# Kernel tuning notes

Measured on AMD Instinct MI355X. Metric: run time of the kernel, lower is better.

Reference implementation:

```python
import jax, jax.numpy as jnp
import numpy as np

B, INPUT_DIM, OUTPUT_DIM, Z_DIM = 32, 2048, 2048, 64
NNZ = 209715


def setup_inputs() -> dict:
    key = jax.random.key(0)
    k_x, k_z, k_w, k_b = jax.random.split(key, 4)
    x = jax.random.normal(k_x, (B, INPUT_DIM), dtype=jnp.float32)
    z = jax.random.normal(k_z, (B, Z_DIM), dtype=jnp.float32)
    W_net = jax.random.normal(k_w, (Z_DIM, NNZ), dtype=jnp.float32) * 0.02
    b_net = jax.random.normal(k_b, (NNZ,), dtype=jnp.float32) * 0.02
    # unique nonzero positions of output_matrix [INPUT_DIM, OUTPUT_DIM]
    rng = np.random.default_rng(0)
    lin = rng.choice(INPUT_DIM * OUTPUT_DIM, size=NNZ, replace=False)
    in_idx = jnp.asarray(lin // OUTPUT_DIM, dtype=jnp.int32)   # rows  -> input dim
    out_idx = jnp.asarray(lin % OUTPUT_DIM, dtype=jnp.int32)   # cols  -> output dim
    return {"x": x, "z": z, "W_net": W_net, "b_net": b_net,
            "in_idx": in_idx, "out_idx": out_idx}


def reference(x, z, W_net, b_net, in_idx, out_idx):
    # hypernetwork: net(z) -> [B, NNZ] matrix entries
    mat_entity = z @ W_net + b_net                      # [B, NNZ]
    # scatter into zero-filled dense matrix: mat[:, out_idx, in_idx] = entries
    mat = jnp.zeros((x.shape[0], OUTPUT_DIM, INPUT_DIM), dtype=x.dtype)
    mat = mat.at[:, out_idx, in_idx].set(mat_entity)    # [B, O, I]
    # batched matvec
    return jnp.einsum('boi,bi->bo', mat, x)             # [B, O]
```

## Files before the change

kernel.cpp:

```cpp
#include <hip/hip_runtime.h>
#include <hip/hip_bf16.h>

#define BATCH   32
#define IN_DIM  2048
#define OUT_DIM 2048
#define ZDIM    64
#define NNZ     209715
#define CAP     160
#define TILES   ((NNZ + 15) / 16)
#define CBLOCKS ((TILES + 3) / 4)
#define NBLK    ((NNZ + 1023) / 1024)

typedef __attribute__((ext_vector_type(8))) short bf16x8;
typedef __attribute__((ext_vector_type(4))) float f32x4;

#define OFF_XT   0
#define OFF_ZBF  262144
#define OFF_CNT  270336
#define OFF_BH   278528
#define OFF_ROW  2375680
#define OFF_E    3214592
#define B_WS_NEEDED (OFF_E + (size_t)OUT_DIM * CAP * BATCH * 2)

__device__ __forceinline__ short f2bf(float f) {
    unsigned u = __float_as_uint(f);
    u += 0x7fffu + ((u >> 16) & 1u);
    return (short)(u >> 16);
}

__global__ __launch_bounds__(256) void prep_x(
    const float* __restrict__ x, const float* __restrict__ z,
    float* __restrict__ xT, short* __restrict__ zbf)
{
    const int idx = blockIdx.x * 256 + threadIdx.x;
    const int b = idx >> 11;
    const int i = idx & 2047;
    xT[i * BATCH + b] = x[idx];
    if (idx < BATCH * ZDIM) zbf[idx] = f2bf(z[idx]);
}

__global__ __launch_bounds__(1024) void hist_blk(
    const int* __restrict__ out_idx, int* __restrict__ bh)
{
    __shared__ int lh[OUT_DIM];
    const int t = threadIdx.x, blk = blockIdx.x;
    lh[t] = 0; lh[t + 1024] = 0;
    __syncthreads();
    const int k = blk * 1024 + t;
    if (k < NNZ) atomicAdd(&lh[out_idx[k]], 1);
    __syncthreads();
    bh[t * 256 + blk]          = lh[t];
    bh[(t + 1024) * 256 + blk] = lh[t + 1024];
}

__global__ __launch_bounds__(256) void colscan(
    int* __restrict__ bh, int* __restrict__ cnt)
{
    const int o    = blockIdx.x * 4 + (threadIdx.x >> 6);
    const int lane = threadIdx.x & 63;
    const int i0   = lane * 4;
    int4 v = *reinterpret_cast<int4*>(bh + o * 256 + i0);
    const int a = (i0 + 0 < NBLK) ? v.x : 0;
    const int b = (i0 + 1 < NBLK) ? v.y : 0;
    const int c = (i0 + 2 < NBLK) ? v.z : 0;
    const int d = (i0 + 3 < NBLK) ? v.w : 0;
    const int s1 = a + b, s2 = s1 + c, tot = s2 + d;
    int inc = tot;
    #pragma unroll
    for (int t = 1; t < 64; t <<= 1) {
        const int n = __shfl_up(inc, t);
        if (lane >= t) inc += n;
    }
    const int exc = inc - tot;
    int4 w; w.x = exc; w.y = exc + a; w.z = exc + s1; w.w = exc + s2;
    *reinterpret_cast<int4*>(bh + o * 256 + i0) = w;
    if (lane == 63) cnt[o] = inc;
}

__global__ __launch_bounds__(1024) void slot_blk(
    const int* __restrict__ out_idx, const int* __restrict__ bh,
    int* __restrict__ rowOf)
{
    __shared__ int lh[OUT_DIM];
    const int t = threadIdx.x, blk = blockIdx.x;
    lh[t] = 0; lh[t + 1024] = 0;
    __syncthreads();
    const int k = blk * 1024 + t;
    if (k < NNZ) {
        const int oi  = out_idx[k];
        const int r   = atomicAdd(&lh[oi], 1);
        const int pos = bh[oi * 256 + blk] + r;
        rowOf[k] = (pos < CAP) ? oi * CAP + pos : -1;
    }
}

__global__ __launch_bounds__(256, 4) void compute_mfma(
    const short* __restrict__ zbf, const float* __restrict__ W,
    const float* __restrict__ bn, const int* __restrict__ in_idx,
    const int* __restrict__ rowOf, const float* __restrict__ xT,
    short* __restrict__ E)
{
    const int lane = threadIdx.x & 63;
    const int m    = lane & 15;
    const int hi   = lane >> 4;
    const int t    = blockIdx.x * 4 + (threadIdx.x >> 6);
    if (t >= TILES) return;
    const int k0 = t * 16;

    bf16x8 zf[2][2];
    #pragma unroll
    for (int bt = 0; bt < 2; ++bt)
        #pragma unroll
        for (int jt = 0; jt < 2; ++jt)
            zf[bt][jt] = *reinterpret_cast<const bf16x8*>(
                zbf + (bt * 16 + m) * ZDIM + jt * 32 + hi * 8);

    const int kA = (k0 + m < NNZ) ? (k0 + m) : (NNZ - 1);
    const float* wp = W + (size_t)(hi * 8) * NNZ + kA;
    float wv[16];
    #pragma unroll
    for (int e = 0; e < 8; ++e) wv[e]     = wp[(size_t)e * NNZ];
    #pragma unroll
    for (int e = 0; e < 8; ++e) wv[8 + e] = wp[(size_t)(32 + e) * NNZ];

    int rowL = -1, iiL = 0; float bnL = 0.f;
    if (lane < 16) {
        const int kk = k0 + lane;
        if (kk < NNZ) {
            rowL = rowOf[kk];
            iiL  = in_idx[kk];
            bnL  = bn[kk];
        }
    }

    union { bf16x8 v; short s[8]; } a0, a1;
    #pragma unroll
    for (int e = 0; e < 8; ++e) { a0.s[e] = f2bf(wv[e]); a1.s[e] = f2bf(wv[8 + e]); }

    f32x4 acc0 = {0.f, 0.f, 0.f, 0.f};
    f32x4 acc1 = {0.f, 0.f, 0.f, 0.f};
    acc0 = __builtin_amdgcn_mfma_f32_16x16x32_bf16(a0.v, zf[0][0], acc0, 0, 0, 0);
    acc0 = __builtin_amdgcn_mfma_f32_16x16x32_bf16(a1.v, zf[0][1], acc0, 0, 0, 0);
    acc1 = __builtin_amdgcn_mfma_f32_16x16x32_bf16(a0.v, zf[1][0], acc1, 0, 0, 0);
    acc1 = __builtin_amdgcn_mfma_f32_16x16x32_bf16(a1.v, zf[1][1], acc1, 0, 0, 0);

    #pragma unroll
    for (int r = 0; r < 4; ++r) {
        const int src  = hi * 4 + r;
        const int row  = __shfl(rowL, src);
        const int ii   = __shfl(iiL, src);
        const float bb = __shfl(bnL, src);
        if (row >= 0) {
            const float x0 = xT[ii * BATCH + m];
            const float x1 = xT[ii * BATCH + 16 + m];
            short* Ep = E + (size_t)row * BATCH;
            Ep[m]      = f2bf((acc0[r] + bb) * x0);
            Ep[16 + m] = f2bf((acc1[r] + bb) * x1);
        }
    }
}

__global__ __launch_bounds__(256) void reduce_bf16(
    const short* __restrict__ E, const int* __restrict__ cnt,
    float* __restrict__ out)
{
    __shared__ float partial[2][BATCH];
    const int wave = threadIdx.x >> 6;
    const int lane = threadIdx.x & 63;
    const int cs   = wave >> 1;
    const int part = wave & 1;
    const int o    = blockIdx.x * 2 + cs;
    const int r  = lane >> 2;
    const int bg = lane & 3;
    const int s = o * CAP;
    int c = cnt[o]; if (c > CAP) c = CAP;
    const int e = s + c;

    float acc[8];
    #pragma unroll
    for (int q = 0; q < 8; ++q) acc[q] = 0.f;

    for (int p = s + part * 16 + r; p < e; p += 32) {
        const uint4 v = *reinterpret_cast<const uint4*>(E + (size_t)p * BATCH + bg * 8);
        const unsigned u[4] = {v.x, v.y, v.z, v.w};
        #pragma unroll
        for (int q = 0; q < 4; ++q) {
            acc[2 * q]     += __uint_as_float((u[q] & 0xFFFFu) << 16);
            acc[2 * q + 1] += __uint_as_float(u[q] & 0xFFFF0000u);
        }
    }

    #pragma unroll
    for (int d = 4; d < 64; d <<= 1)
        #pragma unroll
        for (int q = 0; q < 8; ++q)
            acc[q] += __shfl_xor(acc[q], d);

    if (part == 1 && lane < 4) {
        #pragma unroll
        for (int q = 0; q < 8; ++q) partial[cs][bg * 8 + q] = acc[q];
    }
    __syncthreads();
    if (part == 0 && lane < 4) {
        #pragma unroll
        for (int q = 0; q < 8; ++q)
            out[(bg * 8 + q) * OUT_DIM + o] = acc[q] + partial[cs][bg * 8 + q];
    }
}

__global__ __launch_bounds__(256) void hyper_scatter_kernel(
    const float* __restrict__ x, const float* __restrict__ z,
    const float* __restrict__ W, const float* __restrict__ bn,
    const int* __restrict__ in_idx, const int* __restrict__ out_idx,
    float* __restrict__ out)
{
    __shared__ float zs[BATCH * ZDIM];
    const int tid = threadIdx.x;
    {
        const float4* zg  = reinterpret_cast<const float4*>(z);
        float4*       zsv = reinterpret_cast<float4*>(zs);
        zsv[tid]       = zg[tid];
        zsv[tid + 256] = zg[tid + 256];
    }
    __syncthreads();
    const int k = blockIdx.x * 256 + tid;
    if (k >= NNZ) return;
    float w[ZDIM];
    #pragma unroll
    for (int j = 0; j < ZDIM; ++j) w[j] = W[(size_t)j * NNZ + k];
    const float bk = bn[k];
    const int ii = in_idx[k], oi = out_idx[k];
    const float4* zv = reinterpret_cast<const float4*>(zs);
    #pragma unroll
    for (int b = 0; b < BATCH; ++b) {
        float e = bk;
        #pragma unroll
        for (int j4 = 0; j4 < ZDIM / 4; ++j4) {
            const float4 zz = zv[b * (ZDIM / 4) + j4];
            e = fmaf(zz.x, w[j4 * 4 + 0], e);
            e = fmaf(zz.y, w[j4 * 4 + 1], e);
            e = fmaf(zz.z, w[j4 * 4 + 2], e);
            e = fmaf(zz.w, w[j4 * 4 + 3], e);
        }
        atomicAdd(&out[b * OUT_DIM + oi], e * x[b * IN_DIM + ii]);
    }
}

extern "C" void kernel_launch(void* const* d_in, const int* in_sizes, int n_in,
                              void* d_out, int out_size, void* d_ws, size_t ws_size,
                              hipStream_t stream) {
    const float* x       = (const float*)d_in[0];
    const float* z       = (const float*)d_in[1];
    const float* W       = (const float*)d_in[2];
    const float* bn      = (const float*)d_in[3];
    const int*   in_idx  = (const int*)d_in[4];
    const int*   out_idx = (const int*)d_in[5];
    float*       out     = (float*)d_out;
    char*        ws      = (char*)d_ws;

    if (ws_size >= B_WS_NEEDED) {
        float* xT    = (float*)(ws + OFF_XT);
        short* zbf   = (short*)(ws + OFF_ZBF);
        int*   cnt   = (int*)(ws + OFF_CNT);
        int*   bh    = (int*)(ws + OFF_BH);
        int*   rowOf = (int*)(ws + OFF_ROW);
        short* E     = (short*)(ws + OFF_E);

        prep_x   <<<(BATCH * IN_DIM) / 256, 256, 0, stream>>>(x, z, xT, zbf);
        hist_blk <<<NBLK, 1024, 0, stream>>>(out_idx, bh);
        colscan  <<<OUT_DIM / 4, 256, 0, stream>>>(bh, cnt);
        slot_blk <<<NBLK, 1024, 0, stream>>>(out_idx, bh, rowOf);
        compute_mfma<<<CBLOCKS, 256, 0, stream>>>(zbf, W, bn, in_idx, rowOf, xT, E);
        reduce_bf16 <<<OUT_DIM / 2, 256, 0, stream>>>(E, cnt, out);
    } else {
        hipMemsetAsync(out, 0, (size_t)BATCH * OUT_DIM * sizeof(float), stream);
        const int grid = (NNZ + 255) / 256;
        hyper_scatter_kernel<<<grid, 256, 0, stream>>>(x, z, W, bn, in_idx, out_idx, out);
    }
}
```

Baseline: 46.32 us.

## Fuse x-prep into histogram, process two tiles per wave, one wave per output reduce

Merges the x-transpose/z-conversion kernel into the histogram kernel so one launch goes away. The MFMA compute kernel now handles two 16-entry tiles per wave and issues all W, index and x loads before the matrix ops, to expose more memory-level parallelism. The reduce kernel switches from two waves per output column with an LDS combine and barrier to one wave per column. The costs are higher register pressure in the compute kernel and less parallelism per column in the reduce.

```diff
diff --git a/kernel.cpp b/kernel.cpp
--- a/kernel.cpp
+++ b/kernel.cpp
@@ -8,7 +8,9 @@
 #define NNZ     209715
 #define CAP     160
 #define TILES   ((NNZ + 15) / 16)
-#define CBLOCKS ((TILES + 3) / 4)
+#define TPW     2
+#define CWAVES  ((TILES + TPW - 1) / TPW)
+#define CBLOCKS ((CWAVES + 3) / 4)
 #define NBLK    ((NNZ + 1023) / 1024)
 
 typedef __attribute__((ext_vector_type(8))) short bf16x8;
@@ -28,26 +30,22 @@
     return (short)(u >> 16);
 }
 
-__global__ __launch_bounds__(256) void prep_x(
-    const float* __restrict__ x, const float* __restrict__ z,
+__global__ __launch_bounds__(1024) void hist_prep(
+    const int* __restrict__ out_idx, const float* __restrict__ x,
+    const float* __restrict__ z, int* __restrict__ bh,
     float* __restrict__ xT, short* __restrict__ zbf)
-{
-    const int idx = blockIdx.x * 256 + threadIdx.x;
-    const int b = idx >> 11;
-    const int i = idx & 2047;
-    xT[i * BATCH + b] = x[idx];
-    if (idx < BATCH * ZDIM) zbf[idx] = f2bf(z[idx]);
-}
-
-__global__ __launch_bounds__(1024) void hist_blk(
-    const int* __restrict__ out_idx, int* __restrict__ bh)
 {
     __shared__ int lh[OUT_DIM];
     const int t = threadIdx.x, blk = blockIdx.x;
     lh[t] = 0; lh[t + 1024] = 0;
     __syncthreads();
-    const int k = blk * 1024 + t;
-    if (k < NNZ) atomicAdd(&lh[out_idx[k]], 1);
+    const int gid = blk * 1024 + t;
+    if (gid < BATCH * IN_DIM) {
+        const int b = gid >> 11, i = gid & 2047;
+        xT[i * BATCH + b] = x[gid];
+        if (gid < BATCH * ZDIM) zbf[gid] = f2bf(z[gid]);
+    }
+    if (gid < NNZ) atomicAdd(&lh[out_idx[gid]], 1);
     __syncthreads();
     bh[t * 256 + blk]          = lh[t];
     bh[(t + 1024) * 256 + blk] = lh[t + 1024];
@@ -103,9 +101,9 @@
     const int lane = threadIdx.x & 63;
     const int m    = lane & 15;
     const int hi   = lane >> 4;
-    const int t    = blockIdx.x * 4 + (threadIdx.x >> 6);
-    if (t >= TILES) return;
-    const int k0 = t * 16;
+    const int wid  = blockIdx.x * 4 + (threadIdx.x >> 6);
+    const int t0   = wid * TPW;
+    if (t0 >= TILES) return;
 
     bf16x8 zf[2][2];
     #pragma unroll
@@ -115,47 +113,64 @@
             zf[bt][jt] = *reinterpret_cast<const bf16x8*>(
                 zbf + (bt * 16 + m) * ZDIM + jt * 32 + hi * 8);
 
-    const int kA = (k0 + m < NNZ) ? (k0 + m) : (NNZ - 1);
-    const float* wp = W + (size_t)(hi * 8) * NNZ + kA;
-    float wv[16];
-    #pragma unroll
-    for (int e = 0; e < 8; ++e) wv[e]     = wp[(size_t)e * NNZ];
-    #pragma unroll
-    for (int e = 0; e < 8; ++e) wv[8 + e] = wp[(size_t)(32 + e) * NNZ];
-
-    int rowL = -1, iiL = 0; float bnL = 0.f;
-    if (lane < 16) {
-        const int kk = k0 + lane;
-        if (kk < NNZ) {
-            rowL = rowOf[kk];
-            iiL  = in_idx[kk];
-            bnL  = bn[kk];
-        }
-    }
-
-    union { bf16x8 v; short s[8]; } a0, a1;
-    #pragma unroll
-    for (int e = 0; e < 8; ++e) { a0.s[e] = f2bf(wv[e]); a1.s[e] = f2bf(wv[8 + e]); }
-
-    f32x4 acc0 = {0.f, 0.f, 0.f, 0.f};
-    f32x4 acc1 = {0.f, 0.f, 0.f, 0.f};
-    acc0 = __builtin_amdgcn_mfma_f32_16x16x32_bf16(a0.v, zf[0][0], acc0, 0, 0, 0);
-    acc0 = __builtin_amdgcn_mfma_f32_16x16x32_bf16(a1.v, zf[0][1], acc0, 0, 0, 0);
-    acc1 = __builtin_amdgcn_mfma_f32_16x16x32_bf16(a0.v, zf[1][0], acc1, 0, 0, 0);
-    acc1 = __builtin_amdgcn_mfma_f32_16x16x32_bf16(a1.v, zf[1][1], acc1, 0, 0, 0);
-
-    #pragma unroll
-    for (int r = 0; r < 4; ++r) {
-        const int src  = hi * 4 + r;
-        const int row  = __shfl(rowL, src);
-        const int ii   = __shfl(iiL, src);
-        const float bb = __shfl(bnL, src);
-        if (row >= 0) {
-            const float x0 = xT[ii * BATCH + m];
-            const float x1 = xT[ii * BATCH + 16 + m];
-            short* Ep = E + (size_t)row * BATCH;
-            Ep[m]      = f2bf((acc0[r] + bb) * x0);
-            Ep[16 + m] = f2bf((acc1[r] + bb) * x1);
+    int rowL[2] = {-1, -1}, iiL[2] = {0, 0};
+    float bnL[2] = {0.f, 0.f};
+    #pragma unroll
+    for (int tt = 0; tt < TPW; ++tt) {
+        const int t = t0 + tt;
+        if (t < TILES && lane < 16) {
+            const int kk = t * 16 + lane;
+            if (kk < NNZ) { rowL[tt] = rowOf[kk]; iiL[tt] = in_idx[kk]; bnL[tt] = bn[kk]; }
+        }
+    }
+
+    float wv[2][16];
+    #pragma unroll
+    for (int tt = 0; tt < TPW; ++tt) {
+        const int t  = (t0 + tt < TILES) ? (t0 + tt) : (TILES - 1);
+        const int kA = (t * 16 + m < NNZ) ? (t * 16 + m) : (NNZ - 1);
+        const float* wp = W + (size_t)(hi * 8) * NNZ + kA;
+        #pragma unroll
+        for (int e = 0; e < 8; ++e) wv[tt][e]     = wp[(size_t)e * NNZ];
+        #pragma unroll
+        for (int e = 0; e < 8; ++e) wv[tt][8 + e] = wp[(size_t)(32 + e) * NNZ];
+    }
+
+    int   row_[2][4];
+    float x0_[2][4], x1_[2][4];
+    #pragma unroll
+    for (int tt = 0; tt < TPW; ++tt)
+        #pragma unroll
+        for (int r = 0; r < 4; ++r) {
+            const int src = hi * 4 + r;
+            row_[tt][r] = __shfl(rowL[tt], src);
+            const int ii = __shfl(iiL[tt], src);
+            x0_[tt][r] = xT[ii * BATCH + m];
+            x1_[tt][r] = xT[ii * BATCH + 16 + m];
+        }
+
+    #pragma unroll
+    for (int tt = 0; tt < TPW; ++tt) {
+        union { bf16x8 v; short s[8]; } a0, a1;
+        #pragma unroll
+        for (int e = 0; e < 8; ++e) { a0.s[e] = f2bf(wv[tt][e]); a1.s[e] = f2bf(wv[tt][8 + e]); }
+
+        f32x4 acc0 = {0.f, 0.f, 0.f, 0.f};
+        f32x4 acc1 = {0.f, 0.f, 0.f, 0.f};
+        acc0 = __builtin_amdgcn_mfma_f32_16x16x32_bf16(a0.v, zf[0][0], acc0, 0, 0, 0);
+        acc0 = __builtin_amdgcn_mfma_f32_16x16x32_bf16(a1.v, zf[0][1], acc0, 0, 0, 0);
+        acc1 = __builtin_amdgcn_mfma_f32_16x16x32_bf16(a0.v, zf[1][0], acc1, 0, 0, 0);
+        acc1 = __builtin_amdgcn_mfma_f32_16x16x32_bf16(a1.v, zf[1][1], acc1, 0, 0, 0);
+
+        #pragma unroll
+        for (int r = 0; r < 4; ++r) {
+            const int row = row_[tt][r];
+            if (row >= 0) {
+                const float bb = __shfl(bnL[tt], hi * 4 + r);
+                short* Ep = E + (size_t)row * BATCH;
+                Ep[m]      = f2bf((acc0[r] + bb) * x0_[tt][r]);
+                Ep[16 + m] = f2bf((acc1[r] + bb) * x1_[tt][r]);
+            }
         }
     }
 }
@@ -164,12 +179,8 @@
     const short* __restrict__ E, const int* __restrict__ cnt,
     float* __restrict__ out)
 {
-    __shared__ float partial[2][BATCH];
-    const int wave = threadIdx.x >> 6;
+    const int o    = blockIdx.x * 4 + (threadIdx.x >> 6);
     const int lane = threadIdx.x & 63;
-    const int cs   = wave >> 1;
-    const int part = wave & 1;
-    const int o    = blockIdx.x * 2 + cs;
     const int r  = lane >> 2;
     const int bg = lane & 3;
     const int s = o * CAP;
@@ -180,7 +191,7 @@
     #pragma unroll
     for (int q = 0; q < 8; ++q) acc[q] = 0.f;
 
-    for (int p = s + part * 16 + r; p < e; p += 32) {
+    for (int p = s + r; p < e; p += 16) {
         const uint4 v = *reinterpret_cast<const uint4*>(E + (size_t)p * BATCH + bg * 8);
         const unsigned u[4] = {v.x, v.y, v.z, v.w};
         #pragma unroll
@@ -196,15 +207,10 @@
         for (int q = 0; q < 8; ++q)
             acc[q] += __shfl_xor(acc[q], d);
 
-    if (part == 1 && lane < 4) {
-        #pragma unroll
-        for (int q = 0; q < 8; ++q) partial[cs][bg * 8 + q] = acc[q];
-    }
-    __syncthreads();
-    if (part == 0 && lane < 4) {
+    if (lane < 4) {
         #pragma unroll
         for (int q = 0; q < 8; ++q)
-            out[(bg * 8 + q) * OUT_DIM + o] = acc[q] + partial[cs][bg * 8 + q];
+            out[(bg * 8 + q) * OUT_DIM + o] = acc[q];
     }
 }
 
@@ -266,12 +272,11 @@
         int*   rowOf = (int*)(ws + OFF_ROW);
         short* E     = (short*)(ws + OFF_E);
 
-        prep_x   <<<(BATCH * IN_DIM) / 256, 256, 0, stream>>>(x, z, xT, zbf);
-        hist_blk <<<NBLK, 1024, 0, stream>>>(out_idx, bh);
+        hist_prep<<<NBLK, 1024, 0, stream>>>(out_idx, x, z, bh, xT, zbf);
         colscan  <<<OUT_DIM / 4, 256, 0, stream>>>(bh, cnt);
         slot_blk <<<NBLK, 1024, 0, stream>>>(out_idx, bh, rowOf);
         compute_mfma<<<CBLOCKS, 256, 0, stream>>>(zbf, W, bn, in_idx, rowOf, xT, E);
-        reduce_bf16 <<<OUT_DIM / 2, 256, 0, stream>>>(E, cnt, out);
+        reduce_bf16 <<<OUT_DIM / 4, 256, 0, stream>>>(E, cnt, out);
     } else {
         hipMemsetAsync(out, 0, (size_t)BATCH * OUT_DIM * sizeof(float), stream);
         const int grid = (NNZ + 255) / 256;
```

After: 42.78 us. -7.6%, faster.
